# Kernel optimization log

Hardware: AMD Instinct MI355X
Metric: run time of the kernel (lower is better)

## Reference

```python
import jax, jax.numpy as jnp
import numpy as np

D_MODEL = 1024
NUM_HEADS = 16
D_K = D_MODEL // NUM_HEADS


def setup_inputs() -> dict:
    key = jax.random.key(0)
    ks = jax.random.split(key, 9)
    s = 1.0 / np.sqrt(D_MODEL)
    x = jax.random.normal(ks[0], (4, 2048, D_MODEL), dtype=jnp.float32)
    Wq = jax.random.uniform(ks[1], (D_MODEL, D_MODEL), jnp.float32, -s, s)
    bq = jax.random.uniform(ks[2], (D_MODEL,), jnp.float32, -s, s)
    Wk = jax.random.uniform(ks[3], (D_MODEL, D_MODEL), jnp.float32, -s, s)
    bk = jax.random.uniform(ks[4], (D_MODEL,), jnp.float32, -s, s)
    Wv = jax.random.uniform(ks[5], (D_MODEL, D_MODEL), jnp.float32, -s, s)
    bv = jax.random.uniform(ks[6], (D_MODEL,), jnp.float32, -s, s)
    Wo = jax.random.uniform(ks[7], (D_MODEL, D_MODEL), jnp.float32, -s, s)
    bo = jax.random.uniform(ks[8], (D_MODEL,), jnp.float32, -s, s)
    return {"x": x, "Wq": Wq, "bq": bq, "Wk": Wk, "bk": bk,
            "Wv": Wv, "bv": bv, "Wo": Wo, "bo": bo}


def reference(x, Wq, bq, Wk, bk, Wv, bv, Wo, bo):
    B, S, _ = x.shape
    # Linear projections (torch Linear: x @ W.T + b)
    q = x @ Wq.T + bq
    k = x @ Wk.T + bk
    v = x @ Wv.T + bv
    # [B, H, S, d_k]
    q = q.reshape(B, S, NUM_HEADS, D_K).transpose(0, 2, 1, 3)
    k = k.reshape(B, S, NUM_HEADS, D_K).transpose(0, 2, 1, 3)
    v = v.reshape(B, S, NUM_HEADS, D_K).transpose(0, 2, 1, 3)
    score = jnp.einsum('bhqd,bhkd->bhqk', q, k) / jnp.sqrt(jnp.float32(D_K))
    causal = jnp.tril(jnp.ones((S, S), dtype=bool))  # True = keep
    score = jnp.where(causal[None, None], score, -jnp.inf)
    attn = jax.nn.softmax(score, axis=-1)
    out = jnp.einsum('bhqk,bhkd->bhqd', attn, v)
    out = out.transpose(0, 2, 1, 3).reshape(B, S, D_MODEL)
    return out @ Wo.T + bo
```

## Files before the change

kernel.cpp:

```cpp
#include <hip/hip_runtime.h>
#include <hip/hip_bf16.h>
#include <stdint.h>

#define D_MODEL 1024
#define SEQ     2048
#define BATCH   4
#define NHEAD   16
#define DKH     64
#define MTOT    (BATCH * SEQ)

typedef __bf16 bf16x8 __attribute__((ext_vector_type(8)));
typedef __bf16 bf16x4 __attribute__((ext_vector_type(4)));
typedef float  floatx4 __attribute__((ext_vector_type(4)));
typedef short  s16x4  __attribute__((ext_vector_type(4)));

#define GLOAD_LDS16(gp, lp)                                            \
    __builtin_amdgcn_global_load_lds(                                  \
        (const __attribute__((address_space(1))) unsigned int*)(gp),   \
        (__attribute__((address_space(3))) unsigned int*)(lp), 16, 0, 0)

#define MFMA16(a, b, c) __builtin_amdgcn_mfma_f32_16x16x32_bf16(a, b, c, 0, 0, 0)

#if __has_builtin(__builtin_amdgcn_exp2f)
#define EXP2(x) __builtin_amdgcn_exp2f(x)
#else
#define EXP2(x) exp2f(x)
#endif

static __device__ __forceinline__ floatx4 pv_mfma(s16x4 a, s16x4 b, floatx4 c)
{
#if __has_builtin(__builtin_amdgcn_mfma_f32_16x16x16bf16_1k)
    return __builtin_amdgcn_mfma_f32_16x16x16bf16_1k(a, b, c, 0, 0, 0);
#else
    asm("v_mfma_f32_16x16x16_bf16 %0, %1, %2, %0" : "+v"(c) : "v"(a), "v"(b));
    return c;
#endif
}

__global__ __launch_bounds__(256)
void cvt_x_kernel(const float* __restrict__ src, __bf16* __restrict__ dst)
{
    const int i = (blockIdx.x * 256 + threadIdx.x) * 4;
    floatx4 v = *(const floatx4*)(src + i);
    bf16x4 o;
    o[0] = (__bf16)v[0]; o[1] = (__bf16)v[1]; o[2] = (__bf16)v[2]; o[3] = (__bf16)v[3];
    *(bf16x4*)(dst + i) = o;
}

__global__ __launch_bounds__(256)
void cvt_w3_kernel(const float* __restrict__ Wq, const float* __restrict__ Wk,
                   const float* __restrict__ Wv, __bf16* __restrict__ Wcat)
{
    const int z = blockIdx.y;
    const float* src = (z == 0) ? Wq : ((z == 1) ? Wk : Wv);
    const int i = (blockIdx.x * 256 + threadIdx.x) * 4;
    floatx4 v = *(const floatx4*)(src + i);
    bf16x4 o;
    o[0] = (__bf16)v[0]; o[1] = (__bf16)v[1]; o[2] = (__bf16)v[2]; o[3] = (__bf16)v[3];
    *(bf16x4*)(Wcat + (size_t)z * (D_MODEL * D_MODEL) + i) = o;
}

__global__ __launch_bounds__(256)
void qkv_gemm_kernel(const __bf16* __restrict__ xb, const __bf16* __restrict__ Wcat,
                     const float* __restrict__ bq, const float* __restrict__ bk,
                     const float* __restrict__ bv,
                     __bf16* __restrict__ Q, __bf16* __restrict__ K,
                     __bf16* __restrict__ Vt)
{
    __shared__ __align__(16) char smem_raw[128 * 136 * 2];
    __bf16* As = (__bf16*)smem_raw;
    __bf16* Bs = (__bf16*)(smem_raw + 8192);
    __bf16* Cs = (__bf16*)smem_raw;

    const int t    = threadIdx.x;
    const int w    = t >> 6, l = t & 63, quad = l >> 4, r16 = l & 15;
    const int wm   = w & 1, wn = w >> 1;
    const int m0   = blockIdx.y * 128;
    const int n0   = blockIdx.x * 128;
    const int z    = n0 >> 10;
    const float* bias = (z == 0) ? bq : ((z == 1) ? bk : bv);
    __bf16* outQK     = (z == 0) ? Q  : K;
    const float scale = (z == 0) ? 0.18033688011112042f : 1.0f;

    floatx4 acc[4][4];
#pragma unroll
    for (int i = 0; i < 4; ++i)
#pragma unroll
        for (int j = 0; j < 4; ++j) acc[i][j] = (floatx4){0.f, 0.f, 0.f, 0.f};

    const int c0 = t, c1 = t + 256;
    const __bf16* Ag0 = xb   + (size_t)(m0 + (c0 >> 2)) * 1024 + (c0 & 3) * 8;
    const __bf16* Ag1 = xb   + (size_t)(m0 + (c1 >> 2)) * 1024 + (c1 & 3) * 8;
    const __bf16* Bg0 = Wcat + (size_t)(n0 + (c0 >> 2)) * 1024 + (c0 & 3) * 8;
    const __bf16* Bg1 = Wcat + (size_t)(n0 + (c1 >> 2)) * 1024 + (c1 & 3) * 8;
    unsigned int* lAs = (unsigned int*)As;
    unsigned int* lBs = (unsigned int*)Bs;

    for (int k0 = 0; k0 < 1024; k0 += 32) {
        __syncthreads();
        GLOAD_LDS16(Ag0 + k0, lAs + c0 * 4);
        GLOAD_LDS16(Ag1 + k0, lAs + c1 * 4);
        GLOAD_LDS16(Bg0 + k0, lBs + c0 * 4);
        GLOAD_LDS16(Bg1 + k0, lBs + c1 * 4);
        __syncthreads();

        bf16x8 af[4], bfm[4];
#pragma unroll
        for (int i = 0; i < 4; ++i)
            af[i] = *(const bf16x8*)&As[(wm * 64 + i * 16 + r16) * 32 + quad * 8];
#pragma unroll
        for (int j = 0; j < 4; ++j)
            bfm[j] = *(const bf16x8*)&Bs[(wn * 64 + j * 16 + r16) * 32 + quad * 8];
#pragma unroll
        for (int i = 0; i < 4; ++i)
#pragma unroll
            for (int j = 0; j < 4; ++j)
                acc[i][j] = MFMA16(af[i], bfm[j], acc[i][j]);
    }

    __syncthreads();

    if (z == 2) {
#pragma unroll
        for (int i = 0; i < 4; ++i) {
            const int mb = wm * 64 + i * 16 + quad * 4;
#pragma unroll
            for (int j = 0; j < 4; ++j) {
                const int nl = wn * 64 + j * 16 + r16;
                const float bb = bias[(n0 + nl) & 1023];
                bf16x4 p4;
#pragma unroll
                for (int r = 0; r < 4; ++r) p4[r] = (__bf16)(acc[i][j][r] + bb);
                *(bf16x4*)&Cs[nl * 136 + mb] = p4;
            }
        }
    } else {
#pragma unroll
        for (int i = 0; i < 4; ++i) {
            const int mb = wm * 64 + i * 16 + quad * 4;
#pragma unroll
            for (int j = 0; j < 4; ++j) {
                const int nl = wn * 64 + j * 16 + r16;
                const float bb = bias[(n0 + nl) & 1023];
#pragma unroll
                for (int r = 0; r < 4; ++r)
                    Cs[(mb + r) * 136 + nl] =
                        (__bf16)((acc[i][j][r] + bb) * scale);
            }
        }
    }
    __syncthreads();

    const int b  = m0 >> 11;
    if (z == 2) {
#pragma unroll
        for (int k = 0; k < 8; ++k) {
            const int nl = (t >> 4) + k * 16;
            const int ml = (t & 15) * 8;
            bf16x8 row = *(const bf16x8*)&Cs[nl * 136 + ml];
            const int f = (n0 + nl) & 1023, h = f >> 6, d = f & 63;
            const int s = (m0 & 2047) + ml;
            *(bf16x8*)&Vt[((size_t)((b * 16 + h) * 64 + d) << 11) + s] = row;
        }
    } else {
#pragma unroll
        for (int k = 0; k < 8; ++k) {
            const int ml = (t >> 4) + k * 16;
            const int nl = (t & 15) * 8;
            bf16x8 row = *(const bf16x8*)&Cs[ml * 136 + nl];
            const int f = (n0 + nl) & 1023, h = f >> 6, d = f & 63;
            const int s = (m0 & 2047) + ml;
            *(bf16x8*)&outQK[((size_t)(b * 16 + h) << 17) + ((size_t)s << 6) + d]
                = row;
        }
    }
}

__global__ __launch_bounds__(256)
void out_gemm_kernel(const __bf16* __restrict__ A, const __bf16* __restrict__ Wob,
                     const float* __restrict__ bo, float* __restrict__ out)
{
    __shared__ __align__(16) __bf16 As[128 * 32];
    __shared__ __align__(16) __bf16 Bs[128 * 32];

    const int t    = threadIdx.x;
    const int w    = t >> 6, l = t & 63, quad = l >> 4, r16 = l & 15;
    const int wm   = w & 1, wn = w >> 1;
    const int m0   = blockIdx.y * 128;
    const int n0   = blockIdx.x * 128;

    floatx4 acc[4][4];
#pragma unroll
    for (int i = 0; i < 4; ++i)
#pragma unroll
        for (int j = 0; j < 4; ++j) acc[i][j] = (floatx4){0.f, 0.f, 0.f, 0.f};

    const int c0 = t, c1 = t + 256;
    const __bf16* Ag0 = A   + (size_t)(m0 + (c0 >> 2)) * 1024 + (c0 & 3) * 8;
    const __bf16* Ag1 = A   + (size_t)(m0 + (c1 >> 2)) * 1024 + (c1 & 3) * 8;
    const __bf16* Bg0 = Wob + (size_t)(n0 + (c0 >> 2)) * 1024 + (c0 & 3) * 8;
    const __bf16* Bg1 = Wob + (size_t)(n0 + (c1 >> 2)) * 1024 + (c1 & 3) * 8;
    unsigned int* lAs = (unsigned int*)As;
    unsigned int* lBs = (unsigned int*)Bs;

    for (int k0 = 0; k0 < 1024; k0 += 32) {
        __syncthreads();
        GLOAD_LDS16(Ag0 + k0, lAs + c0 * 4);
        GLOAD_LDS16(Ag1 + k0, lAs + c1 * 4);
        GLOAD_LDS16(Bg0 + k0, lBs + c0 * 4);
        GLOAD_LDS16(Bg1 + k0, lBs + c1 * 4);
        __syncthreads();

        bf16x8 af[4], bfm[4];
#pragma unroll
        for (int i = 0; i < 4; ++i)
            af[i] = *(const bf16x8*)&As[(wm * 64 + i * 16 + r16) * 32 + quad * 8];
#pragma unroll
        for (int j = 0; j < 4; ++j)
            bfm[j] = *(const bf16x8*)&Bs[(wn * 64 + j * 16 + r16) * 32 + quad * 8];
#pragma unroll
        for (int i = 0; i < 4; ++i)
#pragma unroll
            for (int j = 0; j < 4; ++j)
                acc[i][j] = MFMA16(af[i], bfm[j], acc[i][j]);
    }

#pragma unroll
    for (int i = 0; i < 4; ++i) {
        const int mg = m0 + wm * 64 + i * 16 + quad * 4;
#pragma unroll
        for (int j = 0; j < 4; ++j) {
            const int ng = n0 + wn * 64 + j * 16 + r16;
            const float bb = bo[ng];
#pragma unroll
            for (int r = 0; r < 4; ++r)
                out[(size_t)(mg + r) * 1024 + ng] = acc[i][j][r] + bb;
        }
    }
}

__global__ __launch_bounds__(256)
void attn_kernel(const __bf16* __restrict__ Qg, const __bf16* __restrict__ Kg,
                 const __bf16* __restrict__ Vtg, __bf16* __restrict__ O)
{
    __shared__ __align__(16) __bf16 Ks[64 * 72];
    __shared__ __align__(16) __bf16 Vt[64 * 72];

    const int t    = threadIdx.x;
    const int w    = t >> 6, l = t & 63, quad = l >> 4, r16 = l & 15;
    const int bh   = blockIdx.y;
    const int qt   = ((blockIdx.y >> 4) & 1) ? (15 - (int)blockIdx.x)
                                             : (int)blockIdx.x;
    const int q0   = qt * 128;
    const size_t base = (size_t)bh * SEQ * DKH;

    bf16x8 qf[2][2];
#pragma unroll
    for (int mi = 0; mi < 2; ++mi) {
        const int row = q0 + w * 32 + mi * 16 + r16;
        qf[mi][0] = *(const bf16x8*)&Qg[base + (size_t)row * 64 + quad * 8];
        qf[mi][1] = *(const bf16x8*)&Qg[base + (size_t)row * 64 + 32 + quad * 8];
    }

    floatx4 o[2][4];
#pragma unroll
    for (int mi = 0; mi < 2; ++mi)
#pragma unroll
        for (int j = 0; j < 4; ++j) o[mi][j] = (floatx4){0.f, 0.f, 0.f, 0.f};
    float lsum[2] = {0.f, 0.f};

    const int wrow0  = q0 + w * 32;
    const int diagkt = wrow0 >> 6;
    const int nkt    = 2 * qt + 2;
    const int srow   = t >> 3;
    const int sg     = (t & 7) * 8;

    bf16x8 pk[2], pv[2];
#pragma unroll
    for (int it = 0; it < 2; ++it) {
        const int row = it * 32 + srow;
        pk[it] = *(const bf16x8*)&Kg[base + (size_t)row * 64 + sg];
        pv[it] = *(const bf16x8*)&Vtg[base + (size_t)row * 2048 + sg];
    }

    for (int kt = 0; kt < nkt; ++kt) {
        __syncthreads();
#pragma unroll
        for (int it = 0; it < 2; ++it) {
            const int row = it * 32 + srow;
            *(bf16x8*)&Ks[row * 72 + sg] = pk[it];
            *(bf16x8*)&Vt[row * 72 + sg] = pv[it];
        }
        __syncthreads();
        if (kt + 1 < nkt) {
#pragma unroll
            for (int it = 0; it < 2; ++it) {
                const int row = it * 32 + srow;
                pk[it] = *(const bf16x8*)&Kg[base + (size_t)((kt + 1) * 64 + row) * 64 + sg];
                pv[it] = *(const bf16x8*)&Vtg[base + (size_t)row * 2048 + (kt + 1) * 64 + sg];
            }
        }

        if (kt <= diagkt) {
            bf16x8 kf[4][2];
#pragma unroll
            for (int j = 0; j < 4; ++j) {
                kf[j][0] = *(const bf16x8*)&Ks[(j * 16 + r16) * 72 + quad * 8];
                kf[j][1] = *(const bf16x8*)&Ks[(j * 16 + r16) * 72 + 32 + quad * 8];
            }
#pragma unroll
            for (int j = 0; j < 4; ++j) {
                floatx4 z0 = (floatx4){0.f, 0.f, 0.f, 0.f};
                floatx4 z1 = (floatx4){0.f, 0.f, 0.f, 0.f};
                z0 = MFMA16(kf[j][0], qf[0][0], z0);
                z0 = MFMA16(kf[j][1], qf[0][1], z0);
                z1 = MFMA16(kf[j][0], qf[1][0], z1);
                z1 = MFMA16(kf[j][1], qf[1][1], z1);

                bf16x4 pb0, pb1;
                if (kt < diagkt) {
#pragma unroll
                    for (int r = 0; r < 4; ++r) {
                        const float p0 = EXP2(fminf(z0[r], 80.f));
                        const float p1 = EXP2(fminf(z1[r], 80.f));
                        lsum[0] += p0; lsum[1] += p1;
                        pb0[r] = (__bf16)p0; pb1[r] = (__bf16)p1;
                    }
                } else {
                    const int kg  = kt * 64 + j * 16 + quad * 4;
                    const int qg0 = wrow0 + r16;
                    const int qg1 = wrow0 + 16 + r16;
#pragma unroll
                    for (int r = 0; r < 4; ++r) {
                        float p0 = 0.f, p1 = 0.f;
                        if (kg + r <= qg0) p0 = EXP2(fminf(z0[r], 80.f));
                        if (kg + r <= qg1) p1 = EXP2(fminf(z1[r], 80.f));
                        lsum[0] += p0; lsum[1] += p1;
                        pb0[r] = (__bf16)p0; pb1[r] = (__bf16)p1;
                    }
                }
                const s16x4 pa0 = __builtin_bit_cast(s16x4, pb0);
                const s16x4 pa1 = __builtin_bit_cast(s16x4, pb1);
#pragma unroll
                for (int jd = 0; jd < 4; ++jd) {
                    const s16x4 vv =
                        *(const s16x4*)&Vt[(jd * 16 + r16) * 72 + j * 16 + quad * 4];
                    o[0][jd] = pv_mfma(pa0, vv, o[0][jd]);
                    o[1][jd] = pv_mfma(pa1, vv, o[1][jd]);
                }
            }
        }
    }

    float lred[2];
#pragma unroll
    for (int mi = 0; mi < 2; ++mi) {
        float v = lsum[mi];
        v += __shfl_xor(v, 16, 64);
        v += __shfl_xor(v, 32, 64);
        lred[mi] = v;
    }

    const int b = bh >> 4, h = bh & 15;
#pragma unroll
    for (int mi = 0; mi < 2; ++mi)
#pragma unroll
        for (int r = 0; r < 4; ++r) {
            const int qrow = wrow0 + mi * 16 + quad * 4 + r;
            const float lval = __shfl(lred[mi], quad * 4 + r, 64);
            const float inv = 1.f / lval;
#pragma unroll
            for (int jd = 0; jd < 4; ++jd) {
                const int d = jd * 16 + r16;
                O[((size_t)(b * SEQ + qrow) * D_MODEL) + h * 64 + d] =
                    (__bf16)(o[mi][jd][r] * inv);
            }
        }
}

extern "C" void kernel_launch(void* const* d_in, const int* in_sizes, int n_in,
                              void* d_out, int out_size, void* d_ws, size_t ws_size,
                              hipStream_t stream)
{
    (void)in_sizes; (void)n_in; (void)out_size; (void)ws_size;
    const float* x  = (const float*)d_in[0];
    const float* Wq = (const float*)d_in[1];
    const float* bq = (const float*)d_in[2];
    const float* Wk = (const float*)d_in[3];
    const float* bk = (const float*)d_in[4];
    const float* Wv = (const float*)d_in[5];
    const float* bv = (const float*)d_in[6];
    const float* Wo = (const float*)d_in[7];
    const float* bo = (const float*)d_in[8];
    float* out = (float*)d_out;

    const size_t n_elem = (size_t)MTOT * D_MODEL;
    const int    w_n    = D_MODEL * D_MODEL;
    __bf16* Qb  = (__bf16*)d_out;
    __bf16* xb  = Qb + n_elem;
    __bf16* Kb   = (__bf16*)d_ws;
    __bf16* Vtb  = Kb + n_elem;
    __bf16* Ab   = Vtb + n_elem;
    __bf16* Wcat = Ab;
    __bf16* Wob  = Kb;

    cvt_x_kernel<<<MTOT * D_MODEL / 1024, 256, 0, stream>>>(x, xb);
    cvt_w3_kernel<<<dim3(w_n / 1024, 3), 256, 0, stream>>>(Wq, Wk, Wv, Wcat);
    qkv_gemm_kernel<<<dim3(24, 64), 256, 0, stream>>>(xb, Wcat, bq, bk, bv,
                                                      Qb, Kb, Vtb);
    attn_kernel<<<dim3(16, 64), 256, 0, stream>>>(Qb, Kb, Vtb, Ab);
    cvt_x_kernel<<<w_n / 1024, 256, 0, stream>>>(Wo, Wob);
    out_gemm_kernel<<<dim3(8, 64), 256, 0, stream>>>(Ab, Wob, bo, out);
}
```

Measured before the change: 283.6 us.

## Pair causal query tiles per block and double-buffer K/V in LDS

The attention kernel now launches 512-thread blocks, and each block handles two query tiles (qa and 15-qb) that share the same K/V stream. This balances the causal triangle's work across blocks, and each wave owns 16 rows from each tile. K/V staging uses double-buffered LDS with a single barrier per iteration instead of two. The grid is reordered so the batch-head index comes first. Waves on the short tile leave their second MFMA path idle while the long tile is still running, so part of the block sits unused for part of the time.

New measurement: 271.7 us. 1.04x faster.

```diff
diff --git a/kernel.cpp b/kernel.cpp
--- a/kernel.cpp
+++ b/kernel.cpp
@@ -239,28 +239,31 @@
     }
 }
 
-__global__ __launch_bounds__(256)
+__global__ __launch_bounds__(512, 4)
 void attn_kernel(const __bf16* __restrict__ Qg, const __bf16* __restrict__ Kg,
                  const __bf16* __restrict__ Vtg, __bf16* __restrict__ O)
 {
-    __shared__ __align__(16) __bf16 Ks[64 * 72];
-    __shared__ __align__(16) __bf16 Vt[64 * 72];
+    __shared__ __align__(16) __bf16 Ks[2][64 * 72];
+    __shared__ __align__(16) __bf16 Vs[2][64 * 72];
 
     const int t    = threadIdx.x;
     const int w    = t >> 6, l = t & 63, quad = l >> 4, r16 = l & 15;
-    const int bh   = blockIdx.y;
-    const int qt   = ((blockIdx.y >> 4) & 1) ? (15 - (int)blockIdx.x)
-                                             : (int)blockIdx.x;
-    const int q0   = qt * 128;
+    const int bh   = blockIdx.x;
+    const int qb   = blockIdx.y;
+    const int qa   = 15 - qb;
     const size_t base = (size_t)bh * SEQ * DKH;
+    const int g    = w >> 2;
+    const int d0   = 2 * qa + g;
+    const int d1   = 2 * qb + g;
+    const int nkt  = 2 * qa + 2;
+    const int row0 = qa * 128 + w * 16;
+    const int row1 = qb * 128 + w * 16;
 
     bf16x8 qf[2][2];
-#pragma unroll
-    for (int mi = 0; mi < 2; ++mi) {
-        const int row = q0 + w * 32 + mi * 16 + r16;
-        qf[mi][0] = *(const bf16x8*)&Qg[base + (size_t)row * 64 + quad * 8];
-        qf[mi][1] = *(const bf16x8*)&Qg[base + (size_t)row * 64 + 32 + quad * 8];
-    }
+    qf[0][0] = *(const bf16x8*)&Qg[base + (size_t)(row0 + r16) * 64 + quad * 8];
+    qf[0][1] = *(const bf16x8*)&Qg[base + (size_t)(row0 + r16) * 64 + 32 + quad * 8];
+    qf[1][0] = *(const bf16x8*)&Qg[base + (size_t)(row1 + r16) * 64 + quad * 8];
+    qf[1][1] = *(const bf16x8*)&Qg[base + (size_t)(row1 + r16) * 64 + 32 + quad * 8];
 
     floatx4 o[2][4];
 #pragma unroll
@@ -269,44 +272,30 @@
         for (int j = 0; j < 4; ++j) o[mi][j] = (floatx4){0.f, 0.f, 0.f, 0.f};
     float lsum[2] = {0.f, 0.f};
 
-    const int wrow0  = q0 + w * 32;
-    const int diagkt = wrow0 >> 6;
-    const int nkt    = 2 * qt + 2;
-    const int srow   = t >> 3;
-    const int sg     = (t & 7) * 8;
-
-    bf16x8 pk[2], pv[2];
-#pragma unroll
-    for (int it = 0; it < 2; ++it) {
-        const int row = it * 32 + srow;
-        pk[it] = *(const bf16x8*)&Kg[base + (size_t)row * 64 + sg];
-        pv[it] = *(const bf16x8*)&Vtg[base + (size_t)row * 2048 + sg];
-    }
+    const int srow = t >> 3;
+    const int sg   = (t & 7) * 8;
+
+    bf16x8 pk = *(const bf16x8*)&Kg[base + (size_t)srow * 64 + sg];
+    bf16x8 pv = *(const bf16x8*)&Vtg[base + (size_t)srow * 2048 + sg];
 
     for (int kt = 0; kt < nkt; ++kt) {
+        __bf16* ks = Ks[kt & 1];
+        __bf16* vs = Vs[kt & 1];
+        *(bf16x8*)&ks[srow * 72 + sg] = pk;
+        *(bf16x8*)&vs[srow * 72 + sg] = pv;
+        if (kt + 1 < nkt) {
+            pk = *(const bf16x8*)&Kg[base + (size_t)((kt + 1) * 64 + srow) * 64 + sg];
+            pv = *(const bf16x8*)&Vtg[base + (size_t)srow * 2048 + (kt + 1) * 64 + sg];
+        }
         __syncthreads();
-#pragma unroll
-        for (int it = 0; it < 2; ++it) {
-            const int row = it * 32 + srow;
-            *(bf16x8*)&Ks[row * 72 + sg] = pk[it];
-            *(bf16x8*)&Vt[row * 72 + sg] = pv[it];
-        }
-        __syncthreads();
-        if (kt + 1 < nkt) {
-#pragma unroll
-            for (int it = 0; it < 2; ++it) {
-                const int row = it * 32 + srow;
-                pk[it] = *(const bf16x8*)&Kg[base + (size_t)((kt + 1) * 64 + row) * 64 + sg];
-                pv[it] = *(const bf16x8*)&Vtg[base + (size_t)row * 2048 + (kt + 1) * 64 + sg];
-            }
-        }
-
-        if (kt <= diagkt) {
+
+        const bool a0 = (kt <= d0), a1 = (kt <= d1);
+        if (a0) {
             bf16x8 kf[4][2];
 #pragma unroll
             for (int j = 0; j < 4; ++j) {
-                kf[j][0] = *(const bf16x8*)&Ks[(j * 16 + r16) * 72 + quad * 8];
-                kf[j][1] = *(const bf16x8*)&Ks[(j * 16 + r16) * 72 + 32 + quad * 8];
+                kf[j][0] = *(const bf16x8*)&ks[(j * 16 + r16) * 72 + quad * 8];
+                kf[j][1] = *(const bf16x8*)&ks[(j * 16 + r16) * 72 + 32 + quad * 8];
             }
 #pragma unroll
             for (int j = 0; j < 4; ++j) {
@@ -314,39 +303,58 @@
                 floatx4 z1 = (floatx4){0.f, 0.f, 0.f, 0.f};
                 z0 = MFMA16(kf[j][0], qf[0][0], z0);
                 z0 = MFMA16(kf[j][1], qf[0][1], z0);
-                z1 = MFMA16(kf[j][0], qf[1][0], z1);
-                z1 = MFMA16(kf[j][1], qf[1][1], z1);
-
+                if (a1) {
+                    z1 = MFMA16(kf[j][0], qf[1][0], z1);
+                    z1 = MFMA16(kf[j][1], qf[1][1], z1);
+                }
+
+                const int kg = kt * 64 + j * 16 + quad * 4;
                 bf16x4 pb0, pb1;
-                if (kt < diagkt) {
+                if (kt < d0) {
 #pragma unroll
                     for (int r = 0; r < 4; ++r) {
-                        const float p0 = EXP2(fminf(z0[r], 80.f));
-                        const float p1 = EXP2(fminf(z1[r], 80.f));
-                        lsum[0] += p0; lsum[1] += p1;
-                        pb0[r] = (__bf16)p0; pb1[r] = (__bf16)p1;
+                        const float p = EXP2(fminf(z0[r], 80.f));
+                        lsum[0] += p;
+                        pb0[r] = (__bf16)p;
                     }
                 } else {
-                    const int kg  = kt * 64 + j * 16 + quad * 4;
-                    const int qg0 = wrow0 + r16;
-                    const int qg1 = wrow0 + 16 + r16;
+                    const int qg0 = row0 + r16;
 #pragma unroll
                     for (int r = 0; r < 4; ++r) {
-                        float p0 = 0.f, p1 = 0.f;
-                        if (kg + r <= qg0) p0 = EXP2(fminf(z0[r], 80.f));
-                        if (kg + r <= qg1) p1 = EXP2(fminf(z1[r], 80.f));
-                        lsum[0] += p0; lsum[1] += p1;
-                        pb0[r] = (__bf16)p0; pb1[r] = (__bf16)p1;
+                        float p = 0.f;
+                        if (kg + r <= qg0) p = EXP2(fminf(z0[r], 80.f));
+                        lsum[0] += p;
+                        pb0[r] = (__bf16)p;
                     }
                 }
-                const s16x4 pa0 = __builtin_bit_cast(s16x4, pb0);
-                const s16x4 pa1 = __builtin_bit_cast(s16x4, pb1);
+                s16x4 pa0 = __builtin_bit_cast(s16x4, pb0);
+                s16x4 pa1;
+                if (a1) {
+                    if (kt < d1) {
+#pragma unroll
+                        for (int r = 0; r < 4; ++r) {
+                            const float p = EXP2(fminf(z1[r], 80.f));
+                            lsum[1] += p;
+                            pb1[r] = (__bf16)p;
+                        }
+                    } else {
+                        const int qg1 = row1 + r16;
+#pragma unroll
+                        for (int r = 0; r < 4; ++r) {
+                            float p = 0.f;
+                            if (kg + r <= qg1) p = EXP2(fminf(z1[r], 80.f));
+                            lsum[1] += p;
+                            pb1[r] = (__bf16)p;
+                        }
+                    }
+                    pa1 = __builtin_bit_cast(s16x4, pb1);
+                }
 #pragma unroll
                 for (int jd = 0; jd < 4; ++jd) {
                     const s16x4 vv =
-                        *(const s16x4*)&Vt[(jd * 16 + r16) * 72 + j * 16 + quad * 4];
+                        *(const s16x4*)&vs[(jd * 16 + r16) * 72 + j * 16 + quad * 4];
                     o[0][jd] = pv_mfma(pa0, vv, o[0][jd]);
-                    o[1][jd] = pv_mfma(pa1, vv, o[1][jd]);
+                    if (a1) o[1][jd] = pv_mfma(pa1, vv, o[1][jd]);
                 }
             }
         }
@@ -363,10 +371,11 @@
 
     const int b = bh >> 4, h = bh & 15;
 #pragma unroll
-    for (int mi = 0; mi < 2; ++mi)
+    for (int mi = 0; mi < 2; ++mi) {
+        const int rowb = (mi == 0) ? row0 : row1;
 #pragma unroll
         for (int r = 0; r < 4; ++r) {
-            const int qrow = wrow0 + mi * 16 + quad * 4 + r;
+            const int qrow = rowb + quad * 4 + r;
             const float lval = __shfl(lred[mi], quad * 4 + r, 64);
             const float inv = 1.f / lval;
 #pragma unroll
@@ -376,6 +385,7 @@
                     (__bf16)(o[mi][jd][r] * inv);
             }
         }
+    }
 }
 
 extern "C" void kernel_launch(void* const* d_in, const int* in_sizes, int n_in,
@@ -408,7 +418,7 @@
     cvt_w3_kernel<<<dim3(w_n / 1024, 3), 256, 0, stream>>>(Wq, Wk, Wv, Wcat);
     qkv_gemm_kernel<<<dim3(24, 64), 256, 0, stream>>>(xb, Wcat, bq, bk, bv,
                                                       Qb, Kb, Vtb);
-    attn_kernel<<<dim3(16, 64), 256, 0, stream>>>(Qb, Kb, Vtb, Ab);
+    attn_kernel<<<dim3(64, 8), 512, 0, stream>>>(Qb, Kb, Vtb, Ab);
     cvt_x_kernel<<<w_n / 1024, 256, 0, stream>>>(Wo, Wob);
     out_gemm_kernel<<<dim3(8, 64), 256, 0, stream>>>(Ab, Wob, bo, out);
 }
```
